# Kernel optimization log

Hardware: AMD Instinct MI355X
Metric: run time of the kernel (lower is better)

Reference implementation:

```python
import jax, jax.numpy as jnp
import numpy as np

NUM_HEADS = 16
CAPACITY = 512
ROPE_BASE = 10000.0

def _rope_factor(positions, dim):
    # freqs = exp(linspace(0,-1,dim//2) * log(base)), shape (dim//2,)
    freqs = jnp.exp(jnp.linspace(0.0, -1.0, dim // 2) * jnp.log(jnp.float32(ROPE_BASE)))
    angles = positions[..., None] * freqs            # (..., seq, dim//2)
    return jnp.concatenate([jnp.sin(angles), jnp.cos(angles)], axis=-1)  # (..., seq, dim)

def setup_inputs() -> dict:
    key = jax.random.key(0)
    ks = jax.random.split(key, 6)
    B, Sq, Skv, D = 4, 4096, 4096, 1024
    return {
        "query_seq": jax.random.normal(ks[0], (B, Sq, D), jnp.float32),
        "value_seq": jax.random.normal(ks[1], (B, Skv, D), jnp.float32),
        "router_w": jax.random.normal(ks[2], (1, D), jnp.float32) * 0.02,
        "q_w": jax.random.normal(ks[3], (D, D), jnp.float32) * 0.02,
        "kv_w": jax.random.normal(ks[4], (2 * D, D), jnp.float32) * 0.02,
        "out_w": jax.random.normal(ks[5], (D, D), jnp.float32) * 0.02,
    }

def reference(query_seq, value_seq, router_w, q_w, kv_w, out_w):
    B, Sq, D = query_seq.shape
    Skv = value_seq.shape[1]
    H, C = NUM_HEADS, CAPACITY
    d = D // H

    # router + top-k capacity selection over the sequence dim
    rw = jnp.einsum("bsd,od->bs", query_seq, router_w).astype(jnp.float32)  # (B,Sq)
    top_w, top_idx = jax.lax.top_k(rw, C)                                   # (B,C)

    # gather selected queries
    resampled = jnp.take_along_axis(query_seq, top_idx[:, :, None], axis=1)  # (B,C,D)

    q = jnp.einsum("bcd,ed->bce", resampled, q_w)        # (B,C,H*d)
    kv = jnp.einsum("bsd,ed->bse", value_seq, kv_w)      # (B,Skv,2*H*d)
    k, v = jnp.split(kv, 2, axis=-1)

    q = q.reshape(B, C, H, d).transpose(0, 2, 1, 3)      # (B,H,C,d)
    k = k.reshape(B, Skv, H, d).transpose(0, 2, 1, 3)    # (B,H,Skv,d)
    v = v.reshape(B, Skv, H, d).transpose(0, 2, 1, 3)

    # RoPE-style elementwise modulation (faithful to source: x * cat(sin, cos))
    q_pos = top_idx.astype(jnp.float32)[:, None, :]      # (B,1,C)
    q = q * _rope_factor(q_pos, d)                       # (B,H,C,d)
    k_pos = jnp.arange(Skv, dtype=jnp.float32)[None, :]  # (1,Skv)
    k = k * _rope_factor(k_pos, d)[None]                 # broadcast over (B,H)

    # SDPA
    scores = jnp.einsum("bhcd,bhsd->bhcs", q, k) / jnp.sqrt(jnp.float32(d))
    att = jnp.einsum("bhcs,bhsd->bhcd", jax.nn.softmax(scores, axis=-1), v)

    att = att.transpose(0, 2, 1, 3).reshape(B, C, H * d)  # (B,C,D)
    att = jnp.einsum("bce,de->bcd", att, out_w)           # (B,C,D)

    # weighted scatter back to full sequence
    src = att * top_w[:, :, None]
    out = jnp.zeros_like(query_seq).at[jnp.arange(B)[:, None], top_idx].set(src)
    return out
```

## Files before the change

kernel.cpp:

```cpp
#include <hip/hip_runtime.h>
#include <hip/hip_bf16.h>

#define B_  4
#define SQ  4096
#define SKV 4096
#define DM  1024
#define NH  16
#define HD  64
#define CAP 512

#define ASPLIT 4
#define KVPER  (SKV / ASPLIT)
#define AITERS (KVPER / 64)

typedef __attribute__((ext_vector_type(8))) short    short8;
typedef __attribute__((ext_vector_type(8))) __bf16   bf16v8;
typedef __attribute__((ext_vector_type(4))) float    f32x4;
typedef __attribute__((ext_vector_type(4))) unsigned short ushort4v;
typedef __attribute__((ext_vector_type(4))) unsigned int   uint4v;

static __device__ __forceinline__ unsigned short f2bf(float f) {
    unsigned u = __float_as_uint(f);
    u += 0x7FFFu + ((u >> 16) & 1u);
    return (unsigned short)(u >> 16);
}

static __device__ __forceinline__ f32x4 mfma_bf16(short8 a, short8 b, f32x4 c) {
    return __builtin_amdgcn_mfma_f32_16x16x32_bf16(
        __builtin_bit_cast(bf16v8, a), __builtin_bit_cast(bf16v8, b), c, 0, 0, 0);
}

#define GLD16(gp, lp)                                                              \
    __builtin_amdgcn_global_load_lds(                                              \
        (__attribute__((address_space(1))) void*)(gp),                             \
        (__attribute__((address_space(3))) void*)(lp), 16, 0, 0)

__global__ void __launch_bounds__(256) k_convert(const float* __restrict__ in,
                                                 unsigned short* __restrict__ out) {
    size_t i = (size_t)blockIdx.x * 256 + threadIdx.x;
    float4 f = ((const float4*)in)[i];
    ushort4v o = { f2bf(f.x), f2bf(f.y), f2bf(f.z), f2bf(f.w) };
    ((ushort4v*)out)[i] = o;
}

__global__ void __launch_bounds__(256) k_rope(float* __restrict__ tab) {
    int g = blockIdx.x * 256 + threadIdx.x;
    int pos = g >> 6, i = g & 63, j = i & 31;
    float freq = expf(-(float)j * (logf(10000.0f) / 31.0f));
    float ang  = (float)pos * freq;
    tab[g] = (i < 32) ? sinf(ang) : cosf(ang);
}

__global__ void __launch_bounds__(256) k_router(const float* __restrict__ q,
                                                const float* __restrict__ wv,
                                                float* __restrict__ rw) {
    int row  = blockIdx.x * 4 + (threadIdx.x >> 6);
    int lane = threadIdx.x & 63;
    const float* p  = q  + (size_t)row * DM + lane * 16;
    const float* wp = wv + lane * 16;
    float s = 0.f;
#pragma unroll
    for (int j = 0; j < 4; j++) {
        float4 a = ((const float4*)p)[j];
        float4 b = ((const float4*)wp)[j];
        s += a.x * b.x + a.y * b.y + a.z * b.z + a.w * b.w;
    }
#pragma unroll
    for (int m = 32; m > 0; m >>= 1) s += __shfl_xor(s, m, 64);
    if (lane == 0) rw[row] = s;
}

__global__ void __launch_bounds__(1024) k_topk(const float* __restrict__ rw,
                                               int* __restrict__ sel,
                                               float* __restrict__ selw) {
    __shared__ unsigned long long keys[4096];
    int b = blockIdx.x, t = threadIdx.x;
    for (int i = t; i < 4096; i += 1024) {
        float v = rw[b * 4096 + i];
        unsigned u = __float_as_uint(v);
        u = (u & 0x80000000u) ? ~u : (u | 0x80000000u);
        keys[i] = ((unsigned long long)(~u) << 32) | (unsigned)i;
    }
    __syncthreads();
    for (int k = 2; k <= 4096; k <<= 1)
        for (int j = k >> 1; j > 0; j >>= 1) {
            for (int i = t; i < 4096; i += 1024) {
                int ixj = i ^ j;
                if (ixj > i) {
                    bool up = ((i & k) == 0);
                    unsigned long long a = keys[i], c = keys[ixj];
                    if ((a > c) == up) { keys[i] = c; keys[ixj] = a; }
                }
            }
            __syncthreads();
        }
    for (int i = t; i < 512; i += 1024) {
        unsigned idx = (unsigned)(keys[i] & 0xFFFFFFFFu);
        sel[b * 512 + i]  = (int)idx;
        selw[b * 512 + i] = rw[b * 4096 + idx];
    }
}

__global__ void __launch_bounds__(256) k_gather(const float* __restrict__ q,
                                                const int* __restrict__ sel,
                                                unsigned short* __restrict__ out) {
    int row = blockIdx.x;
    int b = row >> 9;
    int s = sel[row];
    const float4* src = (const float4*)(q + ((size_t)b * SQ + s) * DM);
    ushort4v* dst = (ushort4v*)(out + (size_t)row * DM);
    float4 f = src[threadIdx.x];
    ushort4v o = { f2bf(f.x), f2bf(f.y), f2bf(f.z), f2bf(f.w) };
    dst[threadIdx.x] = o;
}

template <int MODE, int BN>
__global__ void __launch_bounds__(256) k_gemm(
    const unsigned short* __restrict__ A,
    const unsigned short* __restrict__ Bw,
    int M, int N, int K,
    const float* __restrict__ rope_tab,
    const int* __restrict__ sel,
    const float* __restrict__ selw,
    unsigned short* __restrict__ ok,
    unsigned short* __restrict__ ov,
    unsigned short* __restrict__ obf,
    float* __restrict__ of) {
    constexpr int TN = BN / 32;
    constexpr int GX = DM / BN;
    __shared__ unsigned short lA[2][128 * 32];
    __shared__ unsigned short lB[2][BN * 32];
    const int tid = threadIdx.x;
    const int w = tid >> 6, lane = tid & 63, quad = lane >> 4, l16 = lane & 15;
    const int wr = w >> 1, wc = w & 1;
    const int nwg = GX * (M >> 7);
    const int bid0 = blockIdx.y * GX + blockIdx.x;
    const int bid  = (bid0 & 7) * (nwg >> 3) + (bid0 >> 3);
    const int mBase = (bid / GX) << 7;
    const int nBase = (bid % GX) * BN + (MODE == 3 ? 1024 : 0);

    f32x4 acc[4][TN] = {};

    auto stage = [&](int buf, int k0) {
#pragma unroll
        for (int is = 0; is < 2; is++) {
            int slot = is * 256 + tid;
            int row = slot >> 2, sc2 = slot & 3;
            int kc = (sc2 - (row >> 1)) & 3;
            const char* ga = (const char*)A + (((size_t)(mBase + row) * K) + k0 + kc * 8) * 2;
            GLD16(ga, (char*)&lA[buf][0] + slot * 16);
        }
#pragma unroll
        for (int is = 0; is < BN / 64; is++) {
            int slot = is * 256 + tid;
            int row = slot >> 2, sc2 = slot & 3;
            int kc = (sc2 - (row >> 1)) & 3;
            const char* gb = (const char*)Bw + (((size_t)(nBase + row) * K) + k0 + kc * 8) * 2;
            GLD16(gb, (char*)&lB[buf][0] + slot * 16);
        }
    };

    const int NT = K >> 5;
    stage(0, 0);
    __syncthreads();

    for (int t = 0; t < NT; t++) {
        if (t + 1 < NT) stage((t + 1) & 1, (t + 1) << 5);
        const unsigned short* bA = &lA[t & 1][0];
        const unsigned short* bB = &lB[t & 1][0];
        short8 af[4], bfr[TN];
#pragma unroll
        for (int tt = 0; tt < 4; tt++) {
            int r = wr * 64 + tt * 16 + l16;
            af[tt] = *(const short8*)&bA[r * 32 + (((quad + (r >> 1)) & 3) * 8)];
        }
#pragma unroll
        for (int tt = 0; tt < TN; tt++) {
            int r = wc * (BN / 2) + tt * 16 + l16;
            bfr[tt] = *(const short8*)&bB[r * 32 + (((quad + (r >> 1)) & 3) * 8)];
        }
#pragma unroll
        for (int tm = 0; tm < 4; tm++)
#pragma unroll
            for (int tn = 0; tn < TN; tn++) {
                if constexpr (MODE == 3)
                    acc[tm][tn] = mfma_bf16(bfr[tn], af[tm], acc[tm][tn]);
                else
                    acc[tm][tn] = mfma_bf16(af[tm], bfr[tn], acc[tm][tn]);
            }
        __syncthreads();
    }

#pragma unroll
    for (int tm = 0; tm < 4; tm++) {
#pragma unroll
        for (int tn = 0; tn < TN; tn++) {
#pragma unroll
            for (int r = 0; r < 4; r++) {
                float v = acc[tm][tn][r];
                if constexpr (MODE == 3) {
                    int n = nBase + wc * (BN / 2) + tn * 16 + quad * 4 + r;
                    int m = mBase + wr * 64 + tm * 16 + l16;
                    int e = n - 1024, h = e >> 6, i = e & 63;
                    int b = m >> 12, s = m & 4095;
                    ov[(((size_t)(b * NH + h) * HD) + i) * SKV + s] = f2bf(v);
                } else {
                    int m = mBase + wr * 64 + tm * 16 + quad * 4 + r;
                    int n = nBase + wc * (BN / 2) + tn * 16 + l16;
                    if constexpr (MODE == 0) {
                        int b = m >> 12, s = m & 4095;
                        int h = n >> 6, i = n & 63;
                        v *= rope_tab[(s << 6) | i];
                        ok[(((size_t)(b * NH + h) * SKV) + s) * HD + i] = f2bf(v);
                    } else if constexpr (MODE == 1) {
                        int b = m >> 9, c = m & 511;
                        int h = n >> 6, i = n & 63;
                        float rp = rope_tab[(sel[m] << 6) | i];
                        obf[(((size_t)(b * NH + h) * CAP) + c) * HD + i] =
                            f2bf(v * rp * 0.18033688011112042f);
                    } else {
                        int b = m >> 9;
                        int s = sel[m];
                        of[(((size_t)b * SQ) + s) * DM + n] = v * selw[m];
                    }
                }
            }
        }
    }
}

template <int C>
static __device__ __forceinline__ void att_step(
    int it, int base, int sr, int sp, int quad, int l16,
    const unsigned short* __restrict__ kb, const unsigned short* __restrict__ vb,
    unsigned short (*lK)[64 * 72], unsigned short (*lV)[64 * 72],
    short8 (&rk)[2], short8 (&rv)[2],
    const short8 (&qf)[2][2],
    f32x4 (&o)[2][4], f32x4 (&lsum)[2], const short8 ones) {
    if (it + 1 < AITERS) {
        unsigned short* dK = &lK[C ^ 1][sr * 72 + sp * 16];
        unsigned short* dV = &lV[C ^ 1][sr * 72 + sp * 16];
        *(short8*)dK       = rk[0];
        *(short8*)(dK + 8) = rk[1];
        *(short8*)dV       = rv[0];
        *(short8*)(dV + 8) = rv[1];
    }
    if (it + 2 < AITERS) {
        int s0 = base + (it + 2) * 64;
        const short8* srck = (const short8*)(kb + (size_t)(s0 + sr) * HD + sp * 16);
        rk[0] = srck[0]; rk[1] = srck[1];
        const short8* srcv = (const short8*)(vb + (size_t)sr * SKV + s0 + sp * 16);
        rv[0] = srcv[0]; rv[1] = srcv[1];
    }

    f32x4 sc[2][4] = {};
    __builtin_amdgcn_s_setprio(1);
#pragma unroll
    for (int tn = 0; tn < 4; tn++) {
        short8 kf0 = *(const short8*)&lK[C][(tn * 16 + l16) * 72 + quad * 8];
        short8 kf1 = *(const short8*)&lK[C][(tn * 16 + l16) * 72 + 32 + quad * 8];
#pragma unroll
        for (int rt = 0; rt < 2; rt++) {
            sc[rt][tn] = mfma_bf16(kf0, qf[rt][0], sc[rt][tn]);
            sc[rt][tn] = mfma_bf16(kf1, qf[rt][1], sc[rt][tn]);
        }
    }
    __builtin_amdgcn_s_setprio(0);
#pragma unroll
    for (int rt = 0; rt < 2; rt++)
#pragma unroll
        for (int tn = 0; tn < 4; tn++)
#pragma unroll
            for (int r = 0; r < 4; r++)
                sc[rt][tn][r] = exp2f(sc[rt][tn][r]);

    short8 pa[2][2];
#pragma unroll
    for (int rt = 0; rt < 2; rt++)
#pragma unroll
        for (int kc = 0; kc < 2; kc++) {
            uint4v wv;
#pragma unroll
            for (int t = 0; t < 4; t++) {
                unsigned pk;
                asm("v_cvt_pk_bf16_f32 %0, %1, %2"
                    : "=v"(pk)
                    : "v"(sc[rt][kc * 2 + (t >> 1)][(t & 1) * 2]),
                      "v"(sc[rt][kc * 2 + (t >> 1)][(t & 1) * 2 + 1]));
                wv[t] = pk;
            }
            pa[rt][kc] = __builtin_bit_cast(short8, wv);
        }

    __builtin_amdgcn_s_setprio(1);
#pragma unroll
    for (int kc = 0; kc < 2; kc++) {
        lsum[0] = mfma_bf16(pa[0][kc], ones, lsum[0]);
        lsum[1] = mfma_bf16(pa[1][kc], ones, lsum[1]);
#pragma unroll
        for (int tn = 0; tn < 4; tn++) {
            const unsigned short* vrow = &lV[C][(size_t)(tn * 16 + l16) * 72];
            uint2 g0 = *(const uint2*)(vrow + kc * 32 + quad * 4);
            uint2 g1 = *(const uint2*)(vrow + kc * 32 + 16 + quad * 4);
            uint4v wv = { g0.x, g0.y, g1.x, g1.y };
            short8 vf = __builtin_bit_cast(short8, wv);
            o[0][tn] = mfma_bf16(pa[0][kc], vf, o[0][tn]);
            o[1][tn] = mfma_bf16(pa[1][kc], vf, o[1][tn]);
        }
    }
    __builtin_amdgcn_s_setprio(0);
    __syncthreads();
}

__global__ void __launch_bounds__(256) k_attention(
    const unsigned short* __restrict__ Q,
    const unsigned short* __restrict__ Kg,
    const unsigned short* __restrict__ Vt,
    float* __restrict__ Opart,
    float* __restrict__ Lpart) {
    __shared__ unsigned short lK[2][64 * 72];
    __shared__ unsigned short lV[2][64 * 72];
    const int bid0 = (blockIdx.z * 64 + blockIdx.y) * 4 + blockIdx.x;
    const int bid  = (bid0 & 7) * 128 + (bid0 >> 3);
    const int bx = bid & 3, bh = (bid >> 2) & 63, z = bid >> 8;
    const int tid = threadIdx.x, w = tid >> 6, lane = tid & 63;
    const int quad = lane >> 4, l16 = lane & 15;
    const int qb = bx * 128 + w * 32;
    const int base = z * KVPER;

    short8 qf[2][2];
#pragma unroll
    for (int rt = 0; rt < 2; rt++) {
        const unsigned short* qp = Q + ((size_t)bh * CAP + qb + rt * 16 + l16) * HD + quad * 8;
        qf[rt][0] = *(const short8*)qp;
        qf[rt][1] = *(const short8*)(qp + 32);
    }

    const unsigned short* kb = Kg + (size_t)bh * SKV * HD;
    const unsigned short* vb = Vt + (size_t)bh * HD * SKV;
    const int sr = tid >> 2, sp = tid & 3;

    f32x4 o[2][4] = {};
    f32x4 lsum[2] = {};
    short8 ones = (short8)0x3F80;

    short8 rk[2], rv[2];
    {
        const short8* srck = (const short8*)(kb + (size_t)(base + sr) * HD + sp * 16);
        rk[0] = srck[0]; rk[1] = srck[1];
        const short8* srcv = (const short8*)(vb + (size_t)sr * SKV + base + sp * 16);
        rv[0] = srcv[0]; rv[1] = srcv[1];
    }
    {
        unsigned short* dK = &lK[0][sr * 72 + sp * 16];
        unsigned short* dV = &lV[0][sr * 72 + sp * 16];
        *(short8*)dK       = rk[0];
        *(short8*)(dK + 8) = rk[1];
        *(short8*)dV       = rv[0];
        *(short8*)(dV + 8) = rv[1];
    }
    {
        int s0 = base + 64;
        const short8* srck = (const short8*)(kb + (size_t)(s0 + sr) * HD + sp * 16);
        rk[0] = srck[0]; rk[1] = srck[1];
        const short8* srcv = (const short8*)(vb + (size_t)sr * SKV + s0 + sp * 16);
        rv[0] = srcv[0]; rv[1] = srcv[1];
    }
    __syncthreads();

    for (int it = 0; it < AITERS; it += 2) {
        att_step<0>(it,     base, sr, sp, quad, l16, kb, vb, lK, lV, rk, rv, qf, o, lsum, ones);
        att_step<1>(it + 1, base, sr, sp, quad, l16, kb, vb, lK, lV, rk, rv, qf, o, lsum, ones);
    }

    float* Ob = Opart + (((size_t)(z * 64 + bh)) * CAP + qb) * HD;
#pragma unroll
    for (int rt = 0; rt < 2; rt++)
#pragma unroll
        for (int tn = 0; tn < 4; tn++)
#pragma unroll
            for (int r = 0; r < 4; r++)
                Ob[(size_t)(rt * 16 + quad * 4 + r) * HD + tn * 16 + l16] = o[rt][tn][r];
    if (l16 == 0) {
#pragma unroll
        for (int rt = 0; rt < 2; rt++)
#pragma unroll
            for (int r = 0; r < 4; r++)
                Lpart[((size_t)(z * 64 + bh)) * CAP + qb + rt * 16 + quad * 4 + r] = lsum[rt][r];
    }
}

__global__ void __launch_bounds__(256) k_combine(
    const float* __restrict__ Opart, const float* __restrict__ Lpart,
    unsigned short* __restrict__ att) {
    int g = blockIdx.x * 256 + threadIdx.x;
    int dall = g & 1023, c = (g >> 10) & 511, b = g >> 19;
    int h = dall >> 6, dd = dall & 63;
    int bh = b * NH + h;
    float os = 0.f, ls = 0.f;
#pragma unroll
    for (int p = 0; p < ASPLIT; p++) {
        os += Opart[(((size_t)(p * 64 + bh)) * CAP + c) * HD + dd];
        ls += Lpart[((size_t)(p * 64 + bh)) * CAP + c];
    }
    att[g] = f2bf(os / ls);
}

extern "C" void kernel_launch(void* const* d_in, const int* in_sizes, int n_in,
                              void* d_out, int out_size, void* d_ws, size_t ws_size,
                              hipStream_t stream) {
    const float* query    = (const float*)d_in[0];
    const float* value    = (const float*)d_in[1];
    const float* router_w = (const float*)d_in[2];
    const float* q_w      = (const float*)d_in[3];
    const float* kv_w     = (const float*)d_in[4];
    const float* out_w    = (const float*)d_in[5];
    float* out = (float*)d_out;

    char* p = (char*)d_ws;
    unsigned short* value_bf = (unsigned short*)p; p += (size_t)B_ * SKV * DM * 2;
    unsigned short* kvw_bf   = (unsigned short*)p; p += (size_t)2 * DM * DM * 2;
    unsigned short* qw_bf    = (unsigned short*)p; p += (size_t)DM * DM * 2;
    unsigned short* ow_bf    = (unsigned short*)p; p += (size_t)DM * DM * 2;
    unsigned short* res_bf   = (unsigned short*)p; p += (size_t)B_ * CAP * DM * 2;
    unsigned short* q_attn   = (unsigned short*)p; p += (size_t)B_ * CAP * DM * 2;
    unsigned short* kbuf     = (unsigned short*)p; p += (size_t)B_ * SKV * DM * 2;
    unsigned short* vbuf     = (unsigned short*)p; p += (size_t)B_ * SKV * DM * 2;
    unsigned short* att_bf   = (unsigned short*)p; p += (size_t)B_ * CAP * DM * 2;
    float* rope_tab = (float*)p; p += (size_t)SKV * HD * 4;
    float* rw       = (float*)p; p += (size_t)B_ * SQ * 4;
    int*   sel      = (int*)p;   p += (size_t)B_ * CAP * 4;
    float* selw     = (float*)p; p += (size_t)B_ * CAP * 4;
    float* Opart = (float*)value_bf;
    float* Lpart = (float*)res_bf;

    hipMemsetAsync(d_out, 0, (size_t)out_size * sizeof(float), stream);

    k_convert<<<B_ * SKV * DM / 1024, 256, 0, stream>>>(value, value_bf);
    k_convert<<<2 * DM * DM / 1024, 256, 0, stream>>>(kv_w, kvw_bf);
    k_convert<<<DM * DM / 1024, 256, 0, stream>>>(q_w, qw_bf);
    k_convert<<<DM * DM / 1024, 256, 0, stream>>>(out_w, ow_bf);
    k_rope<<<SKV * HD / 256, 256, 0, stream>>>(rope_tab);
    k_router<<<B_ * SQ / 4, 256, 0, stream>>>(query, router_w, rw);
    k_topk<<<B_, 1024, 0, stream>>>(rw, sel, selw);
    k_gather<<<B_ * CAP, 256, 0, stream>>>(query, sel, res_bf);

    k_gemm<0, 128><<<dim3(DM / 128, B_ * SKV / 128), 256, 0, stream>>>(
        value_bf, kvw_bf, B_ * SKV, DM, DM, rope_tab, nullptr, nullptr,
        kbuf, nullptr, nullptr, nullptr);
    k_gemm<3, 128><<<dim3(DM / 128, B_ * SKV / 128), 256, 0, stream>>>(
        value_bf, kvw_bf, B_ * SKV, DM, DM, nullptr, nullptr, nullptr,
        nullptr, vbuf, nullptr, nullptr);
    k_gemm<1, 64><<<dim3(DM / 64, B_ * CAP / 128), 256, 0, stream>>>(
        res_bf, qw_bf, B_ * CAP, DM, DM, rope_tab, sel, nullptr,
        nullptr, nullptr, q_attn, nullptr);

    k_attention<<<dim3(CAP / 128, B_ * NH, ASPLIT), 256, 0, stream>>>(
        q_attn, kbuf, vbuf, Opart, Lpart);
    k_combine<<<B_ * CAP * DM / 256, 256, 0, stream>>>(Opart, Lpart, att_bf);

    k_gemm<2, 64><<<dim3(DM / 64, B_ * CAP / 128), 256, 0, stream>>>(
        att_bf, ow_bf, B_ * CAP, DM, DM, nullptr, sel, selw,
        nullptr, nullptr, nullptr, out);
}
```

Baseline: 456.4 us.

## Fuse K and V projection GEMMs into one kernel sharing the A tile

Replaces the two separate K and V projection GEMM launches with one kernel. Each block loads the value-sequence A tile once and multiplies it against both the K and V weight tiles, keeping two accumulator sets. This halves global reads of the large activation and removes one launch. In exchange each block needs twice the accumulator registers and more LDS (three double-buffered tiles), which may lower occupancy.

```diff
diff --git a/kernel.cpp b/kernel.cpp
--- a/kernel.cpp
+++ b/kernel.cpp
@@ -114,6 +114,95 @@
     dst[threadIdx.x] = o;
 }
 
+__global__ void __launch_bounds__(256) k_gemm_kv(
+    const unsigned short* __restrict__ A,
+    const unsigned short* __restrict__ Bw,
+    const float* __restrict__ rope_tab,
+    unsigned short* __restrict__ ok,
+    unsigned short* __restrict__ ov) {
+    __shared__ unsigned short lA [2][128 * 32];
+    __shared__ unsigned short lBk[2][128 * 32];
+    __shared__ unsigned short lBv[2][128 * 32];
+    const int tid = threadIdx.x;
+    const int w = tid >> 6, lane = tid & 63, quad = lane >> 4, l16 = lane & 15;
+    const int wr = w >> 1, wc = w & 1;
+    const int bid0 = blockIdx.y * 8 + blockIdx.x;
+    const int bid  = (bid0 & 7) * 128 + (bid0 >> 3);
+    const int mBase = (bid >> 3) << 7;
+    const int nBase = (bid & 7) << 7;
+
+    f32x4 accK[4][4] = {};
+    f32x4 accV[4][4] = {};
+
+    auto stage = [&](int buf, int k0) {
+#pragma unroll
+        for (int is = 0; is < 2; is++) {
+            int slot = is * 256 + tid;
+            int row = slot >> 2, sc2 = slot & 3;
+            int kc = (sc2 - (row >> 1)) & 3;
+            size_t koff = (size_t)k0 + kc * 8;
+            const char* ga = (const char*)A  + (((size_t)(mBase + row) * DM) + koff) * 2;
+            GLD16(ga, (char*)&lA[buf][0] + slot * 16);
+            const char* gk = (const char*)Bw + (((size_t)(nBase + row) * DM) + koff) * 2;
+            GLD16(gk, (char*)&lBk[buf][0] + slot * 16);
+            const char* gv = (const char*)Bw + (((size_t)(nBase + 1024 + row) * DM) + koff) * 2;
+            GLD16(gv, (char*)&lBv[buf][0] + slot * 16);
+        }
+    };
+
+    stage(0, 0);
+    __syncthreads();
+
+    for (int t = 0; t < DM / 32; t++) {
+        if (t + 1 < DM / 32) stage((t + 1) & 1, (t + 1) << 5);
+        const unsigned short* bA = &lA [t & 1][0];
+        const unsigned short* bK = &lBk[t & 1][0];
+        const unsigned short* bV = &lBv[t & 1][0];
+        short8 af[4], bk[4], bv[4];
+#pragma unroll
+        for (int tt = 0; tt < 4; tt++) {
+            int rA = wr * 64 + tt * 16 + l16;
+            af[tt] = *(const short8*)&bA[rA * 32 + (((quad + (rA >> 1)) & 3) * 8)];
+            int rB = wc * 64 + tt * 16 + l16;
+            bk[tt] = *(const short8*)&bK[rB * 32 + (((quad + (rB >> 1)) & 3) * 8)];
+            bv[tt] = *(const short8*)&bV[rB * 32 + (((quad + (rB >> 1)) & 3) * 8)];
+        }
+#pragma unroll
+        for (int tm = 0; tm < 4; tm++)
+#pragma unroll
+            for (int tn = 0; tn < 4; tn++) {
+                accK[tm][tn] = mfma_bf16(af[tm], bk[tn], accK[tm][tn]);
+                accV[tm][tn] = mfma_bf16(bv[tn], af[tm], accV[tm][tn]);
+            }
+        __syncthreads();
+    }
+
+#pragma unroll
+    for (int tm = 0; tm < 4; tm++)
+#pragma unroll
+        for (int tn = 0; tn < 4; tn++)
+#pragma unroll
+            for (int r = 0; r < 4; r++) {
+                {
+                    float v = accK[tm][tn][r];
+                    int m = mBase + wr * 64 + tm * 16 + quad * 4 + r;
+                    int n = nBase + wc * 64 + tn * 16 + l16;
+                    int b = m >> 12, s = m & 4095;
+                    int h = n >> 6, i = n & 63;
+                    v *= rope_tab[(s << 6) | i];
+                    ok[(((size_t)(b * NH + h) * SKV) + s) * HD + i] = f2bf(v);
+                }
+                {
+                    float v = accV[tm][tn][r];
+                    int e = nBase + wc * 64 + tn * 16 + quad * 4 + r;
+                    int m = mBase + wr * 64 + tm * 16 + l16;
+                    int h = e >> 6, i = e & 63;
+                    int b = m >> 12, s = m & 4095;
+                    ov[(((size_t)(b * NH + h) * HD) + i) * SKV + s] = f2bf(v);
+                }
+            }
+}
+
 template <int MODE, int BN>
 __global__ void __launch_bounds__(256) k_gemm(
     const unsigned short* __restrict__ A,
@@ -122,8 +211,6 @@
     const float* __restrict__ rope_tab,
     const int* __restrict__ sel,
     const float* __restrict__ selw,
-    unsigned short* __restrict__ ok,
-    unsigned short* __restrict__ ov,
     unsigned short* __restrict__ obf,
     float* __restrict__ of) {
     constexpr int TN = BN / 32;
@@ -137,7 +224,7 @@
     const int bid0 = blockIdx.y * GX + blockIdx.x;
     const int bid  = (bid0 & 7) * (nwg >> 3) + (bid0 >> 3);
     const int mBase = (bid / GX) << 7;
-    const int nBase = (bid % GX) * BN + (MODE == 3 ? 1024 : 0);
+    const int nBase = (bid % GX) * BN;
 
     f32x4 acc[4][TN] = {};
 
@@ -182,12 +269,8 @@
 #pragma unroll
         for (int tm = 0; tm < 4; tm++)
 #pragma unroll
-            for (int tn = 0; tn < TN; tn++) {
-                if constexpr (MODE == 3)
-                    acc[tm][tn] = mfma_bf16(bfr[tn], af[tm], acc[tm][tn]);
-                else
-                    acc[tm][tn] = mfma_bf16(af[tm], bfr[tn], acc[tm][tn]);
-            }
+            for (int tn = 0; tn < TN; tn++)
+                acc[tm][tn] = mfma_bf16(af[tm], bfr[tn], acc[tm][tn]);
         __syncthreads();
     }
 
@@ -198,31 +281,18 @@
 #pragma unroll
             for (int r = 0; r < 4; r++) {
                 float v = acc[tm][tn][r];
-                if constexpr (MODE == 3) {
-                    int n = nBase + wc * (BN / 2) + tn * 16 + quad * 4 + r;
-                    int m = mBase + wr * 64 + tm * 16 + l16;
-                    int e = n - 1024, h = e >> 6, i = e & 63;
-                    int b = m >> 12, s = m & 4095;
-                    ov[(((size_t)(b * NH + h) * HD) + i) * SKV + s] = f2bf(v);
+                int m = mBase + wr * 64 + tm * 16 + quad * 4 + r;
+                int n = nBase + wc * (BN / 2) + tn * 16 + l16;
+                if constexpr (MODE == 1) {
+                    int b = m >> 9, c = m & 511;
+                    int h = n >> 6, i = n & 63;
+                    float rp = rope_tab[(sel[m] << 6) | i];
+                    obf[(((size_t)(b * NH + h) * CAP) + c) * HD + i] =
+                        f2bf(v * rp * 0.18033688011112042f);
                 } else {
-                    int m = mBase + wr * 64 + tm * 16 + quad * 4 + r;
-                    int n = nBase + wc * (BN / 2) + tn * 16 + l16;
-                    if constexpr (MODE == 0) {
-                        int b = m >> 12, s = m & 4095;
-                        int h = n >> 6, i = n & 63;
-                        v *= rope_tab[(s << 6) | i];
-                        ok[(((size_t)(b * NH + h) * SKV) + s) * HD + i] = f2bf(v);
-                    } else if constexpr (MODE == 1) {
-                        int b = m >> 9, c = m & 511;
-                        int h = n >> 6, i = n & 63;
-                        float rp = rope_tab[(sel[m] << 6) | i];
-                        obf[(((size_t)(b * NH + h) * CAP) + c) * HD + i] =
-                            f2bf(v * rp * 0.18033688011112042f);
-                    } else {
-                        int b = m >> 9;
-                        int s = sel[m];
-                        of[(((size_t)b * SQ) + s) * DM + n] = v * selw[m];
-                    }
+                    int b = m >> 9;
+                    int s = sel[m];
+                    of[(((size_t)b * SQ) + s) * DM + n] = v * selw[m];
                 }
             }
         }
@@ -445,15 +515,11 @@
     k_topk<<<B_, 1024, 0, stream>>>(rw, sel, selw);
     k_gather<<<B_ * CAP, 256, 0, stream>>>(query, sel, res_bf);
 
-    k_gemm<0, 128><<<dim3(DM / 128, B_ * SKV / 128), 256, 0, stream>>>(
-        value_bf, kvw_bf, B_ * SKV, DM, DM, rope_tab, nullptr, nullptr,
-        kbuf, nullptr, nullptr, nullptr);
-    k_gemm<3, 128><<<dim3(DM / 128, B_ * SKV / 128), 256, 0, stream>>>(
-        value_bf, kvw_bf, B_ * SKV, DM, DM, nullptr, nullptr, nullptr,
-        nullptr, vbuf, nullptr, nullptr);
+    k_gemm_kv<<<dim3(DM / 128, B_ * SKV / 128), 256, 0, stream>>>(
+        value_bf, kvw_bf, rope_tab, kbuf, vbuf);
     k_gemm<1, 64><<<dim3(DM / 64, B_ * CAP / 128), 256, 0, stream>>>(
         res_bf, qw_bf, B_ * CAP, DM, DM, rope_tab, sel, nullptr,
-        nullptr, nullptr, q_attn, nullptr);
+        q_attn, nullptr);
 
     k_attention<<<dim3(CAP / 128, B_ * NH, ASPLIT), 256, 0, stream>>>(
         q_attn, kbuf, vbuf, Opart, Lpart);
@@ -461,5 +527,5 @@
 
     k_gemm<2, 64><<<dim3(DM / 64, B_ * CAP / 128), 256, 0, stream>>>(
         att_bf, ow_bf, B_ * CAP, DM, DM, nullptr, sel, selw,
-        nullptr, nullptr, nullptr, out);
-}
+        nullptr, out);
+}
```

Measured after the change: 442.3 us. -3.1%, faster.
